# Kernel tuning notes

Measured on AMD Instinct MI355X. Metric: run time of the kernel, lower is better.

The kernel has to match this reference:

```python
import jax, jax.numpy as jnp
import numpy as np

B, S, A, C, E, H = 256, 512, 8, 256, 64, 256

def _lin_params(key, din, dout):
    k1, k2 = jax.random.split(key)
    bound = 1.0 / np.sqrt(din)
    w = jax.random.uniform(k1, (din, dout), minval=-bound, maxval=bound, dtype=jnp.float32)
    b = jax.random.uniform(k2, (dout,), minval=-bound, maxval=bound, dtype=jnp.float32)
    return w, b

def setup_inputs() -> dict:
    key = jax.random.key(0)
    ks = jax.random.split(key, 9)
    q = jax.random.normal(ks[0], (B, S, A), dtype=jnp.float32)
    st = jax.random.normal(ks[1], (B, S, C), dtype=jnp.float32)
    w1a, b1a = _lin_params(ks[2], C, H)
    w1b, b1b = _lin_params(ks[3], H, A * E)
    w2a, b2a = _lin_params(ks[4], C, H)
    w2b, b2b = _lin_params(ks[5], H, E)
    wb1, bb1 = _lin_params(ks[6], C, E)
    wb2a, bb2a = _lin_params(ks[7], C, H)
    wb2b, bb2b = _lin_params(ks[8], H, 1)
    return dict(agent_q_values=q, central_states=st,
                w1a=w1a, b1a=b1a, w1b=w1b, b1b=b1b,
                w2a=w2a, b2a=b2a, w2b=w2b, b2b=b2b,
                wb1=wb1, bb1=bb1,
                wb2a=wb2a, bb2a=bb2a, wb2b=wb2b, bb2b=bb2b)

def _mlp(x, wa, ba, wb, bb):
    # Linear -> ELU -> Linear
    h = jax.nn.elu(x @ wa + ba)
    return h @ wb + bb

def reference(agent_q_values, central_states,
              w1a, b1a, w1b, b1b,
              w2a, b2a, w2b, b2b,
              wb1, bb1,
              wb2a, bb2a, wb2b, bb2b):
    bsz, seq, na = agent_q_values.shape
    st = central_states.reshape(-1, C)                      # [N, C]
    q = agent_q_values.reshape(-1, na)                      # [N, A]
    w1 = jnp.abs(_mlp(st, w1a, b1a, w1b, b1b)).reshape(-1, na, E)   # [N, A, E]
    b1 = st @ wb1 + bb1                                     # [N, E]
    w2 = jnp.abs(_mlp(st, w2a, b2a, w2b, b2b))              # [N, E]
    b2 = _mlp(st, wb2a, bb2a, wb2b, bb2b)                   # [N, 1]
    hidden = jax.nn.relu(jnp.einsum('na,nae->ne', q, w1) + b1)      # [N, E]
    joint = jnp.einsum('ne,ne->n', hidden, w2)[:, None] + b2        # [N, 1]
    return joint.reshape(bsz, seq, 1)
```

## Files before the change

### kernel.cpp

```cpp
#include <hip/hip_runtime.h>
#include <math.h>

typedef __bf16 bf16_t;
typedef bf16_t bf16x8 __attribute__((ext_vector_type(8)));
typedef float  floatx4 __attribute__((ext_vector_type(4)));

#define MFMA16(a, b, c) __builtin_amdgcn_mfma_f32_16x16x32_bf16((a), (b), (c), 0, 0, 0)

constexpr int NTOT = 256 * 512;
constexpr int CDIM = 256;

constexpr int N_TILES  = 88;
constexpr int WS_ELEMS = N_TILES * 4096;

__global__ void prep_weights(const float* __restrict__ w1a, const float* __restrict__ w1b,
                             const float* __restrict__ w2a, const float* __restrict__ w2b,
                             const float* __restrict__ wb1, const float* __restrict__ wb2a,
                             bf16_t* __restrict__ ws) {
  int idx = blockIdx.x * 256 + threadIdx.x;
  if (idx >= WS_ELEMS) return;
  int t   = idx >> 12;
  int rel = idx & 4095;
  const float* src; int dout; int ct;
  if      (t < 16) { src = w1a;  dout = 256; ct = t; }
  else if (t < 20) { src = wb1;  dout = 64;  ct = t - 16; }
  else if (t < 52) { src = w1b;  dout = 512; ct = t - 20; }
  else if (t < 68) { src = w2a;  dout = 256; ct = t - 52; }
  else if (t < 72) { src = w2b;  dout = 64;  ct = t - 68; }
  else             { src = wb2a; dout = 256; ct = t - 72; }
  int j    = rel & 7;
  int lane = (rel >> 3) & 63;
  int ks   = rel >> 9;
  int o = ct * 16 + (lane & 15);
  int k = ks * 32 + (lane >> 4) * 8 + j;
  ws[idx] = (bf16_t)src[(size_t)k * dout + o];
}

__global__ __launch_bounds__(256, 2)
void mixing_fused(const float* __restrict__ q,
                  const float* __restrict__ st,
                  const bf16_t* __restrict__ W,
                  const float* __restrict__ b1a, const float* __restrict__ b1b,
                  const float* __restrict__ b2a, const float* __restrict__ b2b,
                  const float* __restrict__ bb1,
                  const float* __restrict__ bb2a,
                  const float* __restrict__ wb2b, const float* __restrict__ bb2b,
                  float* __restrict__ out) {
  __shared__ __align__(16) bf16_t t_s[4][32][36];
  __shared__ __align__(16) float  q_s[4][256];

  const int tid  = threadIdx.x;
  const int wid  = tid >> 6;
  const int lane = tid & 63;
  const int l15  = lane & 15;
  const int quad = lane >> 4;
  const int m0   = blockIdx.x * 128 + wid * 32;

  *(float4*)&q_s[wid][lane * 4] = *(const float4*)(q + (size_t)m0 * 8 + lane * 4);

  bf16x8 sA[2][8];
#pragma unroll
  for (int rt = 0; rt < 2; ++rt) {
    const float* rp = st + (size_t)(m0 + rt * 16 + l15) * CDIM;
#pragma unroll
    for (int ks = 0; ks < 8; ++ks) {
      int k0 = ks * 32 + quad * 8;
      float4 f0 = *(const float4*)(rp + k0);
      float4 f1 = *(const float4*)(rp + k0 + 4);
      bf16x8 v;
      v[0] = (bf16_t)f0.x; v[1] = (bf16_t)f0.y; v[2] = (bf16_t)f0.z; v[3] = (bf16_t)f0.w;
      v[4] = (bf16_t)f1.x; v[5] = (bf16_t)f1.y; v[6] = (bf16_t)f1.z; v[7] = (bf16_t)f1.w;
      sA[rt][ks] = v;
    }
  }

  auto gemmG = [&](int g, int h, const bf16x8 (&A)[2][8], floatx4 (&acc)[2]) {
    const bf16_t* wp = W + (size_t)g * 8192 + h * 4096 + lane * 8;
    bf16x8 b[8];
#pragma unroll
    for (int kk = 0; kk < 8; ++kk)
      b[kk] = *(const bf16x8*)(wp + kk * 512);
    floatx4 z = {0.f, 0.f, 0.f, 0.f};
    acc[0] = z; acc[1] = z;
#pragma unroll
    for (int kk = 0; kk < 8; ++kk) {
      acc[0] = MFMA16(A[0][kk], b[kk], acc[0]);
      acc[1] = MFMA16(A[1][kk], b[kk], acc[1]);
    }
  };

  bf16x8 hA[2][8];

#pragma unroll
  for (int ks = 0; ks < 8; ++ks) {
#pragma unroll
    for (int h = 0; h < 2; ++h) {
      int ct = 2 * ks + h;
      floatx4 acc[2];
      gemmG(ks, h, sA, acc);
      float bias = b1a[ct * 16 + l15];
#pragma unroll
      for (int rt = 0; rt < 2; ++rt)
#pragma unroll
        for (int i = 0; i < 4; ++i) {
          float v = acc[rt][i] + bias;
          v = v > 0.f ? v : (__expf(v) - 1.f);
          t_s[wid][rt * 16 + quad * 4 + i][h * 16 + l15] = (bf16_t)v;
        }
    }
#pragma unroll
    for (int rt = 0; rt < 2; ++rt)
      hA[rt][ks] = *(const bf16x8*)&t_s[wid][rt * 16 + l15][quad * 8];
  }

  floatx4 hid[2][4];
#pragma unroll
  for (int gg = 0; gg < 2; ++gg) {
#pragma unroll
    for (int h = 0; h < 2; ++h) {
      int et = 2 * gg + h;
      floatx4 acc[2];
      gemmG(8 + gg, h, sA, acc);
      float bias = bb1[et * 16 + l15];
      hid[0][et] = acc[0] + bias;
      hid[1][et] = acc[1] + bias;
    }
  }

#pragma unroll 1
  for (int a = 0; a < 8; ++a) {
#pragma unroll
    for (int g2 = 0; g2 < 2; ++g2) {
      const int idx = a * 2 + g2;
#pragma unroll
      for (int h = 0; h < 2; ++h) {
        int ct = a * 4 + g2 * 2 + h;
        const int et = g2 * 2 + h;
        floatx4 acc[2];
        gemmG(10 + idx, h, hA, acc);
        float bias = b1b[ct * 16 + l15];
#pragma unroll
        for (int rt = 0; rt < 2; ++rt)
#pragma unroll
          for (int i = 0; i < 4; ++i) {
            float w1v = fabsf(acc[rt][i] + bias);
            float qv  = q_s[wid][(rt * 16 + quad * 4 + i) * 8 + a];
            hid[rt][et][i] += qv * w1v;
          }
      }
    }
  }
#pragma unroll
  for (int rt = 0; rt < 2; ++rt)
#pragma unroll
    for (int et = 0; et < 4; ++et)
#pragma unroll
      for (int i = 0; i < 4; ++i) hid[rt][et][i] = fmaxf(hid[rt][et][i], 0.f);

#pragma unroll
  for (int ks = 0; ks < 8; ++ks) {
#pragma unroll
    for (int h = 0; h < 2; ++h) {
      int ct = 2 * ks + h;
      floatx4 acc[2];
      gemmG(26 + ks, h, sA, acc);
      float bias = b2a[ct * 16 + l15];
#pragma unroll
      for (int rt = 0; rt < 2; ++rt)
#pragma unroll
        for (int i = 0; i < 4; ++i) {
          float v = acc[rt][i] + bias;
          v = v > 0.f ? v : (__expf(v) - 1.f);
          t_s[wid][rt * 16 + quad * 4 + i][h * 16 + l15] = (bf16_t)v;
        }
    }
#pragma unroll
    for (int rt = 0; rt < 2; ++rt)
      hA[rt][ks] = *(const bf16x8*)&t_s[wid][rt * 16 + l15][quad * 8];
  }

  float pj[2][4] = {{0.f, 0.f, 0.f, 0.f}, {0.f, 0.f, 0.f, 0.f}};
#pragma unroll
  for (int gg = 0; gg < 2; ++gg) {
#pragma unroll
    for (int h = 0; h < 2; ++h) {
      int et = 2 * gg + h;
      floatx4 acc[2];
      gemmG(34 + gg, h, hA, acc);
      float bias = b2b[et * 16 + l15];
#pragma unroll
      for (int rt = 0; rt < 2; ++rt)
#pragma unroll
        for (int i = 0; i < 4; ++i) {
          float w2v = fabsf(acc[rt][i] + bias);
          pj[rt][i] += hid[rt][et][i] * w2v;
        }
    }
  }

  float pb[2][4] = {{0.f, 0.f, 0.f, 0.f}, {0.f, 0.f, 0.f, 0.f}};
#pragma unroll 1
  for (int gg = 0; gg < 8; ++gg) {
#pragma unroll
    for (int h = 0; h < 2; ++h) {
      int ct = 2 * gg + h;
      floatx4 acc[2];
      gemmG(36 + gg, h, sA, acc);
      float bias = bb2a[ct * 16 + l15];
      float wv   = wb2b[ct * 16 + l15];
#pragma unroll
      for (int rt = 0; rt < 2; ++rt)
#pragma unroll
        for (int i = 0; i < 4; ++i) {
          float v = acc[rt][i] + bias;
          v = v > 0.f ? v : (__expf(v) - 1.f);
          pb[rt][i] += v * wv;
        }
    }
  }

  float bb2 = bb2b[0];
#pragma unroll
  for (int rt = 0; rt < 2; ++rt)
#pragma unroll
    for (int i = 0; i < 4; ++i) {
      float v = pj[rt][i] + pb[rt][i];
      v += __shfl_xor(v, 1);
      v += __shfl_xor(v, 2);
      v += __shfl_xor(v, 4);
      v += __shfl_xor(v, 8);
      if (l15 == 0) out[m0 + rt * 16 + quad * 4 + i] = v + bb2;
    }
}

extern "C" void kernel_launch(void* const* d_in, const int* in_sizes, int n_in,
                              void* d_out, int out_size, void* d_ws, size_t ws_size,
                              hipStream_t stream) {
  const float* q    = (const float*)d_in[0];
  const float* st   = (const float*)d_in[1];
  const float* w1a  = (const float*)d_in[2];
  const float* b1a  = (const float*)d_in[3];
  const float* w1b  = (const float*)d_in[4];
  const float* b1b  = (const float*)d_in[5];
  const float* w2a  = (const float*)d_in[6];
  const float* b2a  = (const float*)d_in[7];
  const float* w2b  = (const float*)d_in[8];
  const float* b2b  = (const float*)d_in[9];
  const float* wb1  = (const float*)d_in[10];
  const float* bb1  = (const float*)d_in[11];
  const float* wb2a = (const float*)d_in[12];
  const float* bb2a = (const float*)d_in[13];
  const float* wb2b = (const float*)d_in[14];
  const float* bb2b = (const float*)d_in[15];
  bf16_t* W = (bf16_t*)d_ws;

  hipLaunchKernelGGL(prep_weights, dim3((WS_ELEMS + 255) / 256), dim3(256), 0, stream,
                     w1a, w1b, w2a, w2b, wb1, wb2a, W);
  hipLaunchKernelGGL(mixing_fused, dim3(NTOT / 128), dim3(256), 0, stream,
                     q, st, W, b1a, b1b, b2a, b2b, bb1, bb2a, wb2b, bb2b, (float*)d_out);
}
```

Before: 366.4 us.

## Double-buffer weight fragment loads across GEMM tiles in register ping-pong

Splits the weight-tile load from the MFMA compute and uses two register buffers (B0/B1), so the next tile's global weight fragments are fetched while the current tile is multiplied. The prefetch chains across all stages, including the boundaries between phases. The aim is to hide global and L2 load latency behind the MFMA work. In exchange it holds 8 more bf16x8 registers live, which could cost occupancy or cause spills under launch_bounds(256,2).

```diff
diff --git a/kernel.cpp b/kernel.cpp
--- a/kernel.cpp
+++ b/kernel.cpp
@@ -74,12 +74,13 @@
     }
   }
 
-  auto gemmG = [&](int g, int h, const bf16x8 (&A)[2][8], floatx4 (&acc)[2]) {
+  auto LD = [&](bf16x8 (&b)[8], int g, int h) {
     const bf16_t* wp = W + (size_t)g * 8192 + h * 4096 + lane * 8;
-    bf16x8 b[8];
 #pragma unroll
     for (int kk = 0; kk < 8; ++kk)
       b[kk] = *(const bf16x8*)(wp + kk * 512);
+  };
+  auto GEMM = [&](const bf16x8 (&A)[2][8], const bf16x8 (&b)[8], floatx4 (&acc)[2]) {
     floatx4 z = {0.f, 0.f, 0.f, 0.f};
     acc[0] = z; acc[1] = z;
 #pragma unroll
@@ -89,23 +90,39 @@
     }
   };
 
+  bf16x8 B0[8], B1[8];
+  LD(B0, 0, 0);
+
   bf16x8 hA[2][8];
 
 #pragma unroll
   for (int ks = 0; ks < 8; ++ks) {
-#pragma unroll
-    for (int h = 0; h < 2; ++h) {
-      int ct = 2 * ks + h;
-      floatx4 acc[2];
-      gemmG(ks, h, sA, acc);
-      float bias = b1a[ct * 16 + l15];
-#pragma unroll
-      for (int rt = 0; rt < 2; ++rt)
-#pragma unroll
-        for (int i = 0; i < 4; ++i) {
-          float v = acc[rt][i] + bias;
-          v = v > 0.f ? v : (__expf(v) - 1.f);
-          t_s[wid][rt * 16 + quad * 4 + i][h * 16 + l15] = (bf16_t)v;
+    LD(B1, ks, 1);
+    {
+      float bias = b1a[(2 * ks) * 16 + l15];
+      floatx4 acc[2];
+      GEMM(sA, B0, acc);
+#pragma unroll
+      for (int rt = 0; rt < 2; ++rt)
+#pragma unroll
+        for (int i = 0; i < 4; ++i) {
+          float v = acc[rt][i] + bias;
+          v = v > 0.f ? v : (__expf(v) - 1.f);
+          t_s[wid][rt * 16 + quad * 4 + i][l15] = (bf16_t)v;
+        }
+    }
+    LD(B0, (ks < 7) ? ks + 1 : 8, 0);
+    {
+      float bias = b1a[(2 * ks + 1) * 16 + l15];
+      floatx4 acc[2];
+      GEMM(sA, B1, acc);
+#pragma unroll
+      for (int rt = 0; rt < 2; ++rt)
+#pragma unroll
+        for (int i = 0; i < 4; ++i) {
+          float v = acc[rt][i] + bias;
+          v = v > 0.f ? v : (__expf(v) - 1.f);
+          t_s[wid][rt * 16 + quad * 4 + i][16 + l15] = (bf16_t)v;
         }
     }
 #pragma unroll
@@ -116,38 +133,76 @@
   floatx4 hid[2][4];
 #pragma unroll
   for (int gg = 0; gg < 2; ++gg) {
-#pragma unroll
-    for (int h = 0; h < 2; ++h) {
-      int et = 2 * gg + h;
-      floatx4 acc[2];
-      gemmG(8 + gg, h, sA, acc);
-      float bias = bb1[et * 16 + l15];
-      hid[0][et] = acc[0] + bias;
-      hid[1][et] = acc[1] + bias;
+    LD(B1, 8 + gg, 1);
+    {
+      float bias = bb1[(2 * gg) * 16 + l15];
+      floatx4 acc[2];
+      GEMM(sA, B0, acc);
+      hid[0][2 * gg] = acc[0] + bias;
+      hid[1][2 * gg] = acc[1] + bias;
+    }
+    LD(B0, (gg < 1) ? 9 : 10, 0);
+    {
+      float bias = bb1[(2 * gg + 1) * 16 + l15];
+      floatx4 acc[2];
+      GEMM(sA, B1, acc);
+      hid[0][2 * gg + 1] = acc[0] + bias;
+      hid[1][2 * gg + 1] = acc[1] + bias;
     }
   }
 
 #pragma unroll 1
   for (int a = 0; a < 8; ++a) {
-#pragma unroll
-    for (int g2 = 0; g2 < 2; ++g2) {
-      const int idx = a * 2 + g2;
-#pragma unroll
-      for (int h = 0; h < 2; ++h) {
-        int ct = a * 4 + g2 * 2 + h;
-        const int et = g2 * 2 + h;
-        floatx4 acc[2];
-        gemmG(10 + idx, h, hA, acc);
-        float bias = b1b[ct * 16 + l15];
-#pragma unroll
-        for (int rt = 0; rt < 2; ++rt)
-#pragma unroll
-          for (int i = 0; i < 4; ++i) {
-            float w1v = fabsf(acc[rt][i] + bias);
-            float qv  = q_s[wid][(rt * 16 + quad * 4 + i) * 8 + a];
-            hid[rt][et][i] += qv * w1v;
-          }
-      }
+    float qv[2][4];
+#pragma unroll
+    for (int rt = 0; rt < 2; ++rt)
+#pragma unroll
+      for (int i = 0; i < 4; ++i)
+        qv[rt][i] = q_s[wid][(rt * 16 + quad * 4 + i) * 8 + a];
+
+    LD(B1, 10 + 2 * a, 1);
+    {
+      float bias = b1b[(4 * a + 0) * 16 + l15];
+      floatx4 acc[2];
+      GEMM(hA, B0, acc);
+#pragma unroll
+      for (int rt = 0; rt < 2; ++rt)
+#pragma unroll
+        for (int i = 0; i < 4; ++i)
+          hid[rt][0][i] += qv[rt][i] * fabsf(acc[rt][i] + bias);
+    }
+    LD(B0, 11 + 2 * a, 0);
+    {
+      float bias = b1b[(4 * a + 1) * 16 + l15];
+      floatx4 acc[2];
+      GEMM(hA, B1, acc);
+#pragma unroll
+      for (int rt = 0; rt < 2; ++rt)
+#pragma unroll
+        for (int i = 0; i < 4; ++i)
+          hid[rt][1][i] += qv[rt][i] * fabsf(acc[rt][i] + bias);
+    }
+    LD(B1, 11 + 2 * a, 1);
+    {
+      float bias = b1b[(4 * a + 2) * 16 + l15];
+      floatx4 acc[2];
+      GEMM(hA, B0, acc);
+#pragma unroll
+      for (int rt = 0; rt < 2; ++rt)
+#pragma unroll
+        for (int i = 0; i < 4; ++i)
+          hid[rt][2][i] += qv[rt][i] * fabsf(acc[rt][i] + bias);
+    }
+    LD(B0, (a < 7) ? 12 + 2 * a : 26, 0);
+    {
+      float bias = b1b[(4 * a + 3) * 16 + l15];
+      floatx4 acc[2];
+      GEMM(hA, B1, acc);
+#pragma unroll
+      for (int rt = 0; rt < 2; ++rt)
+#pragma unroll
+        for (int i = 0; i < 4; ++i)
+          hid[rt][3][i] += qv[rt][i] * fabsf(acc[rt][i] + bias);
     }
   }
 #pragma unroll
@@ -159,19 +214,32 @@
 
 #pragma unroll
   for (int ks = 0; ks < 8; ++ks) {
-#pragma unroll
-    for (int h = 0; h < 2; ++h) {
-      int ct = 2 * ks + h;
-      floatx4 acc[2];
-      gemmG(26 + ks, h, sA, acc);
-      float bias = b2a[ct * 16 + l15];
-#pragma unroll
-      for (int rt = 0; rt < 2; ++rt)
-#pragma unroll
-        for (int i = 0; i < 4; ++i) {
-          float v = acc[rt][i] + bias;
-          v = v > 0.f ? v : (__expf(v) - 1.f);
-          t_s[wid][rt * 16 + quad * 4 + i][h * 16 + l15] = (bf16_t)v;
+    LD(B1, 26 + ks, 1);
+    {
+      float bias = b2a[(2 * ks) * 16 + l15];
+      floatx4 acc[2];
+      GEMM(sA, B0, acc);
+#pragma unroll
+      for (int rt = 0; rt < 2; ++rt)
+#pragma unroll
+        for (int i = 0; i < 4; ++i) {
+          float v = acc[rt][i] + bias;
+          v = v > 0.f ? v : (__expf(v) - 1.f);
+          t_s[wid][rt * 16 + quad * 4 + i][l15] = (bf16_t)v;
+        }
+    }
+    LD(B0, (ks < 7) ? 27 + ks : 34, 0);
+    {
+      float bias = b2a[(2 * ks + 1) * 16 + l15];
+      floatx4 acc[2];
+      GEMM(sA, B1, acc);
+#pragma unroll
+      for (int rt = 0; rt < 2; ++rt)
+#pragma unroll
+        for (int i = 0; i < 4; ++i) {
+          float v = acc[rt][i] + bias;
+          v = v > 0.f ? v : (__expf(v) - 1.f);
+          t_s[wid][rt * 16 + quad * 4 + i][16 + l15] = (bf16_t)v;
         }
     }
 #pragma unroll
@@ -179,42 +247,63 @@
       hA[rt][ks] = *(const bf16x8*)&t_s[wid][rt * 16 + l15][quad * 8];
   }
 
-  float pj[2][4] = {{0.f, 0.f, 0.f, 0.f}, {0.f, 0.f, 0.f, 0.f}};
+  float p[2][4] = {{0.f, 0.f, 0.f, 0.f}, {0.f, 0.f, 0.f, 0.f}};
 #pragma unroll
   for (int gg = 0; gg < 2; ++gg) {
-#pragma unroll
-    for (int h = 0; h < 2; ++h) {
-      int et = 2 * gg + h;
-      floatx4 acc[2];
-      gemmG(34 + gg, h, hA, acc);
-      float bias = b2b[et * 16 + l15];
-#pragma unroll
-      for (int rt = 0; rt < 2; ++rt)
-#pragma unroll
-        for (int i = 0; i < 4; ++i) {
-          float w2v = fabsf(acc[rt][i] + bias);
-          pj[rt][i] += hid[rt][et][i] * w2v;
-        }
-    }
-  }
-
-  float pb[2][4] = {{0.f, 0.f, 0.f, 0.f}, {0.f, 0.f, 0.f, 0.f}};
+    LD(B1, 34 + gg, 1);
+    {
+      float bias = b2b[(2 * gg) * 16 + l15];
+      floatx4 acc[2];
+      GEMM(hA, B0, acc);
+#pragma unroll
+      for (int rt = 0; rt < 2; ++rt)
+#pragma unroll
+        for (int i = 0; i < 4; ++i)
+          p[rt][i] += hid[rt][2 * gg][i] * fabsf(acc[rt][i] + bias);
+    }
+    LD(B0, (gg < 1) ? 35 : 36, 0);
+    {
+      float bias = b2b[(2 * gg + 1) * 16 + l15];
+      floatx4 acc[2];
+      GEMM(hA, B1, acc);
+#pragma unroll
+      for (int rt = 0; rt < 2; ++rt)
+#pragma unroll
+        for (int i = 0; i < 4; ++i)
+          p[rt][i] += hid[rt][2 * gg + 1][i] * fabsf(acc[rt][i] + bias);
+    }
+  }
+
 #pragma unroll 1
   for (int gg = 0; gg < 8; ++gg) {
-#pragma unroll
-    for (int h = 0; h < 2; ++h) {
-      int ct = 2 * gg + h;
-      floatx4 acc[2];
-      gemmG(36 + gg, h, sA, acc);
-      float bias = bb2a[ct * 16 + l15];
-      float wv   = wb2b[ct * 16 + l15];
-#pragma unroll
-      for (int rt = 0; rt < 2; ++rt)
-#pragma unroll
-        for (int i = 0; i < 4; ++i) {
-          float v = acc[rt][i] + bias;
-          v = v > 0.f ? v : (__expf(v) - 1.f);
-          pb[rt][i] += v * wv;
+    LD(B1, 36 + gg, 1);
+    {
+      float bias = bb2a[(2 * gg) * 16 + l15];
+      float wv   = wb2b[(2 * gg) * 16 + l15];
+      floatx4 acc[2];
+      GEMM(sA, B0, acc);
+#pragma unroll
+      for (int rt = 0; rt < 2; ++rt)
+#pragma unroll
+        for (int i = 0; i < 4; ++i) {
+          float v = acc[rt][i] + bias;
+          v = v > 0.f ? v : (__expf(v) - 1.f);
+          p[rt][i] += v * wv;
+        }
+    }
+    LD(B0, (gg < 7) ? 37 + gg : 43, 0);
+    {
+      float bias = bb2a[(2 * gg + 1) * 16 + l15];
+      float wv   = wb2b[(2 * gg + 1) * 16 + l15];
+      floatx4 acc[2];
+      GEMM(sA, B1, acc);
+#pragma unroll
+      for (int rt = 0; rt < 2; ++rt)
+#pragma unroll
+        for (int i = 0; i < 4; ++i) {
+          float v = acc[rt][i] + bias;
+          v = v > 0.f ? v : (__expf(v) - 1.f);
+          p[rt][i] += v * wv;
         }
     }
   }
@@ -224,7 +313,7 @@
   for (int rt = 0; rt < 2; ++rt)
 #pragma unroll
     for (int i = 0; i < 4; ++i) {
-      float v = pj[rt][i] + pb[rt][i];
+      float v = p[rt][i];
       v += __shfl_xor(v, 1);
       v += __shfl_xor(v, 2);
       v += __shfl_xor(v, 4);
```

New measurement: 356.9 us. 1.03x faster.
